# Optimization experiments

Measured on AMD Instinct MI355X. Metric: run time of the kernel, lower is better.

## Reference

```python
import jax, jax.numpy as jnp
import numpy as np

N, A, B, NRBF, HID = 64, 256, 128, 32, 32


def setup_inputs() -> dict:
    key = jax.random.key(0)
    ks = jax.random.split(key, 8)
    return {
        "t": jax.random.normal(ks[0], (1,), jnp.float32),
        "r": jax.random.normal(ks[1], (N, A, B, 3), jnp.float32),
        "rbfs": jax.random.uniform(ks[2], (N, A, B, NRBF), jnp.float32),
        "f_old": jax.random.normal(ks[3], (N, A, 3), jnp.float32),
        "W1": jax.random.normal(ks[4], (NRBF, HID), jnp.float32) / np.sqrt(NRBF),
        "b1": jnp.zeros((HID,), jnp.float32),
        "W2": jax.random.normal(ks[5], (HID, 1), jnp.float32) / np.sqrt(HID),
        "b2": jnp.zeros((1,), jnp.float32),
    }


def reference(t, r, rbfs, f_old, W1, b1, W2, b2):
    # scalar gate from radial basis features: [n, a, b, 1]
    h = jax.nn.silu(rbfs @ W1 + b1)
    s = h @ W2 + b2
    # einsum('ofi, nabf, nai -> nabo', levi_civita, r, f_old) is exactly the
    # cross product (r x f_old) broadcast over the neighbor axis b.
    rc = jnp.cross(r, f_old[:, :, None, :])  # [n, a, b, 3]
    # gate and reduce over neighbors (dim 2)
    return (s * rc).sum(axis=2)  # [n, a, 3]
```

## Files before the change

kernel.cpp:

```cpp
#include <hip/hip_runtime.h>


#define NRBF 32
#define HID  32

typedef __attribute__((ext_vector_type(8))) short bf16x8;
typedef __attribute__((ext_vector_type(4))) float f32x4;

__device__ __forceinline__ void split_bf16(float x, short& hi, short& lo) {
    unsigned u  = __builtin_bit_cast(unsigned, x);
    unsigned hu = u & 0xFFFF0000u;
    hi = (short)(hu >> 16);
    float l = x - __builtin_bit_cast(float, hu);
    lo = (short)(__builtin_bit_cast(unsigned, l) >> 16);
}

__global__ __launch_bounds__(256, 4) void mbconv_mfma(
    const float* __restrict__ r,
    const float* __restrict__ rbfs,
    const float* __restrict__ f_old,
    const float* __restrict__ W1,
    const float* __restrict__ b1,
    const float* __restrict__ W2,
    const float* __restrict__ b2,
    float* __restrict__ out)
{
    const int t    = threadIdx.x;
    const int wave = t >> 6;
    const int l    = t & 63;
    const int lo4  = l & 15;
    const int hi2  = l >> 4;

    const int  grp    = __builtin_amdgcn_readfirstlane((blockIdx.x << 1) | (wave >> 1));
    const int  nb     = (wave & 1) << 6;
    const long p_base = (long)grp * 128 + nb;

    const float4* rb4 = reinterpret_cast<const float4*>(rbfs);
    float4 stg[8];
    #pragma unroll
    for (int T = 0; T < 4; ++T) {
        const long row = (p_base + T * 16 + lo4) * (NRBF / 4) + hi2 * 2;
        stg[2 * T + 0] = rb4[row];
        stg[2 * T + 1] = rb4[row + 1];
    }
    const long pr = (p_base + l) * 3;
    const float r0 = r[pr + 0], r1 = r[pr + 1], r2 = r[pr + 2];
    const float f0 = f_old[grp * 3 + 0], f1 = f_old[grp * 3 + 1], f2 = f_old[grp * 3 + 2];

    bf16x8 a_hi[2], a_lo[2];
    #pragma unroll
    for (int H = 0; H < 2; ++H) {
        #pragma unroll
        for (int e = 0; e < 8; ++e) {
            const float w = W1[(hi2 * 8 + e) * HID + H * 16 + lo4];
            short h, lw; split_bf16(w, h, lw);
            a_hi[H][e] = h; a_lo[H][e] = lw;
        }
    }

    const float4 b1v0 = *reinterpret_cast<const float4*>(b1 + hi2 * 4);
    const float4 b1v1 = *reinterpret_cast<const float4*>(b1 + 16 + hi2 * 4);
    const float4 w2v0 = *reinterpret_cast<const float4*>(W2 + hi2 * 4);
    const float4 w2v1 = *reinterpret_cast<const float4*>(W2 + 16 + hi2 * 4);
    const float b2v = b2[0];

    float s_arr[4];
    #pragma unroll
    for (int T = 0; T < 4; ++T) {
        const float xv[8] = { stg[2*T].x, stg[2*T].y, stg[2*T].z, stg[2*T].w,
                              stg[2*T+1].x, stg[2*T+1].y, stg[2*T+1].z, stg[2*T+1].w };
        bf16x8 bhi, blo;
        #pragma unroll
        for (int e = 0; e < 8; ++e) {
            short h, lw; split_bf16(xv[e], h, lw);
            bhi[e] = h; blo[e] = lw;
        }
        float ps = 0.f;
        #pragma unroll
        for (int H = 0; H < 2; ++H) {
            f32x4 acc = f32x4{0.f, 0.f, 0.f, 0.f};
            acc = __builtin_amdgcn_mfma_f32_16x16x32_bf16(a_hi[H], bhi, acc, 0, 0, 0);
            acc = __builtin_amdgcn_mfma_f32_16x16x32_bf16(a_hi[H], blo, acc, 0, 0, 0);
            acc = __builtin_amdgcn_mfma_f32_16x16x32_bf16(a_lo[H], bhi, acc, 0, 0, 0);
            const float4 b1v = H ? b1v1 : b1v0;
            const float4 w2v = H ? w2v1 : w2v0;
            #pragma unroll
            for (int q = 0; q < 4; ++q) {
                const float h  = acc[q] + ((const float*)&b1v)[q];
                const float ex = __expf(-h);
                const float sl = h * __builtin_amdgcn_rcpf(1.f + ex);
                ps = fmaf(sl, ((const float*)&w2v)[q], ps);
            }
        }
        ps += __shfl_xor(ps, 16);
        ps += __shfl_xor(ps, 32);
        s_arr[T] = ps + b2v;
    }
    const float s_own = hi2 == 0 ? s_arr[0] : hi2 == 1 ? s_arr[1] : hi2 == 2 ? s_arr[2] : s_arr[3];

    float cx = (r1 * f2 - r2 * f1) * s_own;
    float cy = (r2 * f0 - r0 * f2) * s_own;
    float cz = (r0 * f1 - r1 * f0) * s_own;
    #pragma unroll
    for (int off = 32; off > 0; off >>= 1) {
        cx += __shfl_down(cx, off);
        cy += __shfl_down(cy, off);
        cz += __shfl_down(cz, off);
    }

    __shared__ float red[4][3];
    if (l == 0) { red[wave][0] = cx; red[wave][1] = cy; red[wave][2] = cz; }
    __syncthreads();
    if (t < 2) {
        const long g = ((long)blockIdx.x << 1) | t;
        out[g * 3 + 0] = red[2 * t][0] + red[2 * t + 1][0];
        out[g * 3 + 1] = red[2 * t][1] + red[2 * t + 1][1];
        out[g * 3 + 2] = red[2 * t][2] + red[2 * t + 1][2];
    }
}

extern "C" void kernel_launch(void* const* d_in, const int* in_sizes, int n_in,
                              void* d_out, int out_size, void* d_ws, size_t ws_size,
                              hipStream_t stream) {
    const float* r     = (const float*)d_in[1];
    const float* rbfs  = (const float*)d_in[2];
    const float* f_old = (const float*)d_in[3];
    const float* W1    = (const float*)d_in[4];
    const float* b1    = (const float*)d_in[5];
    const float* W2    = (const float*)d_in[6];
    const float* b2    = (const float*)d_in[7];
    float* out = (float*)d_out;

    const int NA = in_sizes[3] / 3;
    const int blocks = NA / 2;
    mbconv_mfma<<<blocks, 256, 0, stream>>>(r, rbfs, f_old, W1, b1, W2, b2, out);
}
```

Baseline: 50.90 us.

## Use persistent grid-stride waves, one atom group per wave, no LDS reduction

The kernel now launches a fixed grid of 1024 blocks. Each wave loops over atom groups in grid-stride fashion and handles both 64-neighbor halves of a group itself, so the shared-memory reduction and block barrier are gone. The W1 bf16 split and the bias loads are amortized across several groups per wave. The cost is that each wave processes its two halves serially, which gives less memory-level parallelism per group and may expose more load latency.

New measurement: 69.34 us. +36.2%, slower.

```diff
diff --git a/kernel.cpp b/kernel.cpp
--- a/kernel.cpp
+++ b/kernel.cpp
@@ -23,29 +23,14 @@
     const float* __restrict__ b1,
     const float* __restrict__ W2,
     const float* __restrict__ b2,
-    float* __restrict__ out)
+    float* __restrict__ out,
+    int NA)
 {
     const int t    = threadIdx.x;
     const int wave = t >> 6;
     const int l    = t & 63;
     const int lo4  = l & 15;
     const int hi2  = l >> 4;
-
-    const int  grp    = __builtin_amdgcn_readfirstlane((blockIdx.x << 1) | (wave >> 1));
-    const int  nb     = (wave & 1) << 6;
-    const long p_base = (long)grp * 128 + nb;
-
-    const float4* rb4 = reinterpret_cast<const float4*>(rbfs);
-    float4 stg[8];
-    #pragma unroll
-    for (int T = 0; T < 4; ++T) {
-        const long row = (p_base + T * 16 + lo4) * (NRBF / 4) + hi2 * 2;
-        stg[2 * T + 0] = rb4[row];
-        stg[2 * T + 1] = rb4[row + 1];
-    }
-    const long pr = (p_base + l) * 3;
-    const float r0 = r[pr + 0], r1 = r[pr + 1], r2 = r[pr + 2];
-    const float f0 = f_old[grp * 3 + 0], f1 = f_old[grp * 3 + 1], f2 = f_old[grp * 3 + 2];
 
     bf16x8 a_hi[2], a_lo[2];
     #pragma unroll
@@ -57,65 +42,83 @@
             a_hi[H][e] = h; a_lo[H][e] = lw;
         }
     }
-
     const float4 b1v0 = *reinterpret_cast<const float4*>(b1 + hi2 * 4);
     const float4 b1v1 = *reinterpret_cast<const float4*>(b1 + 16 + hi2 * 4);
     const float4 w2v0 = *reinterpret_cast<const float4*>(W2 + hi2 * 4);
     const float4 w2v1 = *reinterpret_cast<const float4*>(W2 + 16 + hi2 * 4);
     const float b2v = b2[0];
 
-    float s_arr[4];
-    #pragma unroll
-    for (int T = 0; T < 4; ++T) {
-        const float xv[8] = { stg[2*T].x, stg[2*T].y, stg[2*T].z, stg[2*T].w,
-                              stg[2*T+1].x, stg[2*T+1].y, stg[2*T+1].z, stg[2*T+1].w };
-        bf16x8 bhi, blo;
+    const float4* rb4 = reinterpret_cast<const float4*>(rbfs);
+    const int wid = (blockIdx.x << 2) | wave;
+    const int nw  = gridDim.x << 2;
+
+    for (int g0 = wid; g0 < NA; g0 += nw) {
+        const int g = __builtin_amdgcn_readfirstlane(g0);
+        const float f0 = f_old[g * 3 + 0], f1 = f_old[g * 3 + 1], f2 = f_old[g * 3 + 2];
+        float cx = 0.f, cy = 0.f, cz = 0.f;
+
         #pragma unroll
-        for (int e = 0; e < 8; ++e) {
-            short h, lw; split_bf16(xv[e], h, lw);
-            bhi[e] = h; blo[e] = lw;
+        for (int half = 0; half < 2; ++half) {
+            const long p_base = (long)g * 128 + half * 64;
+
+            float4 stg[8];
+            #pragma unroll
+            for (int T = 0; T < 4; ++T) {
+                const long row = (p_base + T * 16 + lo4) * (NRBF / 4) + hi2 * 2;
+                stg[2 * T + 0] = rb4[row];
+                stg[2 * T + 1] = rb4[row + 1];
+            }
+            const long pr = (p_base + l) * 3;
+            const float r0 = r[pr + 0], r1 = r[pr + 1], r2 = r[pr + 2];
+
+            float s_arr[4];
+            #pragma unroll
+            for (int T = 0; T < 4; ++T) {
+                const float xv[8] = { stg[2*T].x, stg[2*T].y, stg[2*T].z, stg[2*T].w,
+                                      stg[2*T+1].x, stg[2*T+1].y, stg[2*T+1].z, stg[2*T+1].w };
+                bf16x8 bhi, blo;
+                #pragma unroll
+                for (int e = 0; e < 8; ++e) {
+                    short h, lw; split_bf16(xv[e], h, lw);
+                    bhi[e] = h; blo[e] = lw;
+                }
+                float ps = 0.f;
+                #pragma unroll
+                for (int H = 0; H < 2; ++H) {
+                    f32x4 acc = f32x4{0.f, 0.f, 0.f, 0.f};
+                    acc = __builtin_amdgcn_mfma_f32_16x16x32_bf16(a_hi[H], bhi, acc, 0, 0, 0);
+                    acc = __builtin_amdgcn_mfma_f32_16x16x32_bf16(a_hi[H], blo, acc, 0, 0, 0);
+                    acc = __builtin_amdgcn_mfma_f32_16x16x32_bf16(a_lo[H], bhi, acc, 0, 0, 0);
+                    const float4 b1v = H ? b1v1 : b1v0;
+                    const float4 w2v = H ? w2v1 : w2v0;
+                    #pragma unroll
+                    for (int q = 0; q < 4; ++q) {
+                        const float h  = acc[q] + ((const float*)&b1v)[q];
+                        const float ex = __expf(-h);
+                        const float sl = h * __builtin_amdgcn_rcpf(1.f + ex);
+                        ps = fmaf(sl, ((const float*)&w2v)[q], ps);
+                    }
+                }
+                ps += __shfl_xor(ps, 16);
+                ps += __shfl_xor(ps, 32);
+                s_arr[T] = ps + b2v;
+            }
+            const float s_own = hi2 == 0 ? s_arr[0] : hi2 == 1 ? s_arr[1]
+                              : hi2 == 2 ? s_arr[2] : s_arr[3];
+
+            cx = fmaf(r1 * f2 - r2 * f1, s_own, cx);
+            cy = fmaf(r2 * f0 - r0 * f2, s_own, cy);
+            cz = fmaf(r0 * f1 - r1 * f0, s_own, cz);
         }
-        float ps = 0.f;
+
         #pragma unroll
-        for (int H = 0; H < 2; ++H) {
-            f32x4 acc = f32x4{0.f, 0.f, 0.f, 0.f};
-            acc = __builtin_amdgcn_mfma_f32_16x16x32_bf16(a_hi[H], bhi, acc, 0, 0, 0);
-            acc = __builtin_amdgcn_mfma_f32_16x16x32_bf16(a_hi[H], blo, acc, 0, 0, 0);
-            acc = __builtin_amdgcn_mfma_f32_16x16x32_bf16(a_lo[H], bhi, acc, 0, 0, 0);
-            const float4 b1v = H ? b1v1 : b1v0;
-            const float4 w2v = H ? w2v1 : w2v0;
-            #pragma unroll
-            for (int q = 0; q < 4; ++q) {
-                const float h  = acc[q] + ((const float*)&b1v)[q];
-                const float ex = __expf(-h);
-                const float sl = h * __builtin_amdgcn_rcpf(1.f + ex);
-                ps = fmaf(sl, ((const float*)&w2v)[q], ps);
-            }
+        for (int off = 1; off < 64; off <<= 1) {
+            cx += __shfl_xor(cx, off);
+            cy += __shfl_xor(cy, off);
+            cz += __shfl_xor(cz, off);
         }
-        ps += __shfl_xor(ps, 16);
-        ps += __shfl_xor(ps, 32);
-        s_arr[T] = ps + b2v;
-    }
-    const float s_own = hi2 == 0 ? s_arr[0] : hi2 == 1 ? s_arr[1] : hi2 == 2 ? s_arr[2] : s_arr[3];
-
-    float cx = (r1 * f2 - r2 * f1) * s_own;
-    float cy = (r2 * f0 - r0 * f2) * s_own;
-    float cz = (r0 * f1 - r1 * f0) * s_own;
-    #pragma unroll
-    for (int off = 32; off > 0; off >>= 1) {
-        cx += __shfl_down(cx, off);
-        cy += __shfl_down(cy, off);
-        cz += __shfl_down(cz, off);
-    }
-
-    __shared__ float red[4][3];
-    if (l == 0) { red[wave][0] = cx; red[wave][1] = cy; red[wave][2] = cz; }
-    __syncthreads();
-    if (t < 2) {
-        const long g = ((long)blockIdx.x << 1) | t;
-        out[g * 3 + 0] = red[2 * t][0] + red[2 * t + 1][0];
-        out[g * 3 + 1] = red[2 * t][1] + red[2 * t + 1][1];
-        out[g * 3 + 2] = red[2 * t][2] + red[2 * t + 1][2];
+        if (l < 3)
+            out[(long)g * 3 + l] = (l == 0) ? cx : (l == 1) ? cy : cz;
     }
 }
 
@@ -132,6 +135,6 @@
     float* out = (float*)d_out;
 
     const int NA = in_sizes[3] / 3;
-    const int blocks = NA / 2;
-    mbconv_mfma<<<blocks, 256, 0, stream>>>(r, rbfs, f_old, W1, b1, W2, b2, out);
+    const int blocks = 1024;
+    mbconv_mfma<<<blocks, 256, 0, stream>>>(r, rbfs, f_old, W1, b1, W2, b2, out, NA);
 }
```
